# Kernel optimization log

Measured on AMD Instinct MI355X. Metric: run time of the kernel, lower is better.

Reference implementation:

```python
import jax, jax.numpy as jnp
import numpy as np

N_NODES = 50000
N_EDGES = 800000
D = 128
N_GRAPHS = 64
N_CLASSES = 10


def setup_inputs() -> dict:
    key = jax.random.key(0)
    ks = jax.random.split(key, 10)
    x = jax.random.normal(ks[0], (N_NODES, D), dtype=jnp.float32)
    edge_index = jax.random.randint(ks[1], (2, N_EDGES), 0, N_NODES, dtype=jnp.int64)
    batch = jnp.sort(jax.random.randint(ks[2], (N_NODES,), 0, N_GRAPHS, dtype=jnp.int64))
    s = 1.0 / np.sqrt(D)
    W1a = jax.random.uniform(ks[3], (D, D), jnp.float32, -s, s)
    W1b = jax.random.uniform(ks[4], (D, D), jnp.float32, -s, s)
    W2a = jax.random.uniform(ks[5], (D, D), jnp.float32, -s, s)
    W2b = jax.random.uniform(ks[6], (D, D), jnp.float32, -s, s)
    Wfc = jax.random.uniform(ks[7], (D, N_CLASSES), jnp.float32, -s, s)
    return {
        "x": x, "edge_index": edge_index, "batch": batch,
        "W1a": W1a, "b1a": jnp.zeros((D,), jnp.float32),
        "W1b": W1b, "b1b": jnp.zeros((D,), jnp.float32),
        "W2a": W2a, "b2a": jnp.zeros((D,), jnp.float32),
        "W2b": W2b, "b2b": jnp.zeros((D,), jnp.float32),
        "Wfc": Wfc, "bfc": jnp.zeros((N_CLASSES,), jnp.float32),
    }


def _gin_conv(x, src, dst, Wa, ba, Wb, bb):
    # sum aggregation of neighbor messages x[src] into dst (eps = 0)
    agg = jax.ops.segment_sum(x[src], dst, num_segments=N_NODES)
    h = x + agg  # (1 + eps) * x + sum_{j->i} x_j
    h = jax.nn.relu(h @ Wa + ba)
    h = jax.nn.relu(h @ Wb + bb)
    return h


def reference(x, edge_index, batch, W1a, b1a, W1b, b1b, W2a, b2a, W2b, b2b, Wfc, bfc):
    src, dst = edge_index[0], edge_index[1]
    h = _gin_conv(x, src, dst, W1a, b1a, W1b, b1b)
    h = _gin_conv(h, src, dst, W2a, b2a, W2b, b2b)
    # global mean pool over graphs
    sums = jax.ops.segment_sum(h, batch, num_segments=N_GRAPHS)
    counts = jax.ops.segment_sum(jnp.ones((h.shape[0], 1), h.dtype), batch, num_segments=N_GRAPHS)
    pooled = sums / jnp.maximum(counts, 1.0)
    logits = pooled @ Wfc + bfc
    return jax.nn.sigmoid(logits)
```

## Files before the change

### kernel.cpp

```cpp
#include <hip/hip_runtime.h>

#define NN 50000
#define NE 800000
#define DF 128
#define NG 64
#define NC 10
#define NBK 98
#define PART_CHUNK 4096
#define PART_GRID 196
#define ACAP 12288
#define FINE_CAP 12288
#define RT 136

typedef short bf16x8 __attribute__((ext_vector_type(8)));
typedef float f32x4  __attribute__((ext_vector_type(4)));

__device__ __forceinline__ void atomAddF(float* p, float v) {
  __hip_atomic_fetch_add(p, v, __ATOMIC_RELAXED, __HIP_MEMORY_SCOPE_AGENT);
}
__device__ __forceinline__ float b2f(unsigned short u) {
  union { unsigned int i; float f; } v; v.i = (unsigned int)u << 16; return v.f;
}
__device__ __forceinline__ unsigned int f2b(float f) {
  unsigned int i = __float_as_uint(f);
  return (i + 0x7fffu + ((i >> 16) & 1u)) >> 16;
}

__global__ __launch_bounds__(256) void k_cast(const float* __restrict__ x,
                                              unsigned short* __restrict__ xb)
{
  const int i = blockIdx.x * 256 + threadIdx.x;
  if (i * 4 >= NN * DF) return;
  const float4 v = reinterpret_cast<const float4*>(x)[i];
  uint2 o;
  o.x = f2b(v.x) | (f2b(v.y) << 16);
  o.y = f2b(v.z) | (f2b(v.w) << 16);
  reinterpret_cast<uint2*>(xb)[i] = o;
}

__global__ __launch_bounds__(256) void k_prepw(const float* __restrict__ W0,
                                               const float* __restrict__ W1,
                                               const float* __restrict__ W2,
                                               const float* __restrict__ W3,
                                               unsigned short* __restrict__ Wt)
{
  const int o = blockIdx.x * 256 + threadIdx.x;
  if (o >= 4 * 2048) return;
  const int mat = o >> 11;
  const float* W = (mat == 0) ? W0 : (mat == 1) ? W1 : (mat == 2) ? W2 : W3;
  const int rem = o & 2047;
  const int n  = rem >> 4;
  const int k0 = (rem & 15) * 8;
  unsigned int u[8];
#pragma unroll
  for (int j = 0; j < 8; ++j) u[j] = f2b(W[(size_t)(k0 + j) * DF + n]);
  uint4 p;
  p.x = u[0] | (u[1] << 16);
  p.y = u[2] | (u[3] << 16);
  p.z = u[4] | (u[5] << 16);
  p.w = u[6] | (u[7] << 16);
  *reinterpret_cast<uint4*>(Wt + (size_t)mat * DF * DF + (size_t)n * DF + k0) = p;
}

__global__ __launch_bounds__(256) void k_part(const int* __restrict__ src,
                                              const int* __restrict__ dst,
                                              int* __restrict__ cnt_b,
                                              unsigned int* __restrict__ arena)
{
  __shared__ unsigned int stage[PART_CHUNK];
  __shared__ int lhist[128], lcnt[128], lcur[128], gbase[128];
  const int tid = threadIdx.x;
  const int e0  = blockIdx.x * PART_CHUNK;
  const int nE  = min(PART_CHUNK, NE - e0);

  for (int i = tid; i < 128; i += 256) lhist[i] = 0;
  __syncthreads();

  unsigned int pk[16];
  int bk[16];
#pragma unroll
  for (int i = 0; i < 16; ++i) {
    const int e = e0 + i * 256 + tid;
    if (e < NE) {
      const int d = dst[e];
      const int s = src[e];
      const int b = d >> 9;
      bk[i] = b;
      pk[i] = ((unsigned int)b << 25) | ((unsigned int)(d & 511) << 16) | (unsigned int)s;
      atomicAdd(&lhist[b], 1);
    } else {
      bk[i] = -1;
    }
  }
  __syncthreads();
  for (int i = tid; i < 128; i += 256) lcnt[i] = lhist[i];
  __syncthreads();
  for (int off = 1; off < 128; off <<= 1) {
    int v = 0;
    if (tid < 128 && tid >= off) v = lhist[tid - off];
    __syncthreads();
    if (tid < 128) lhist[tid] += v;
    __syncthreads();
  }
  if (tid < 128) lcur[tid] = lhist[tid] - lcnt[tid];
  __syncthreads();
#pragma unroll
  for (int i = 0; i < 16; ++i) {
    if (bk[i] >= 0) {
      const int pos = atomicAdd(&lcur[bk[i]], 1);
      stage[pos] = pk[i];
    }
  }
  __syncthreads();
  if (tid < NBK) {
    const int c = lcnt[tid];
    if (c > 0) gbase[tid] = atomicAdd(&cnt_b[tid], c);
  }
  __syncthreads();
  for (int idx = tid; idx < nE; idx += 256) {
    const unsigned int p = stage[idx];
    const int b = (int)(p >> 25);
    const int loff = lhist[b] - lcnt[b];
    arena[(size_t)b * ACAP + gbase[b] + (idx - loff)] = p;
  }
}

__global__ __launch_bounds__(128) void k_bscan(const int* __restrict__ cnt_b,
                                               int* __restrict__ base_b,
                                               int* __restrict__ rs)
{
  __shared__ int sm[128];
  const int t = threadIdx.x;
  const int v = (t < NBK) ? cnt_b[t] : 0;
  sm[t] = v;
  __syncthreads();
  for (int off = 1; off < 128; off <<= 1) {
    int u = (t >= off) ? sm[t - off] : 0;
    __syncthreads();
    sm[t] += u;
    __syncthreads();
  }
  base_b[t] = sm[t] - v;
  if (t == NBK - 1) rs[NN] = sm[t];
}

__global__ __launch_bounds__(256) void k_fine(const unsigned int* __restrict__ arena,
                                              const int* __restrict__ cnt_b,
                                              const int* __restrict__ base_b,
                                              int* __restrict__ rs,
                                              int* __restrict__ es)
{
  __shared__ int hist[512], offs[512], pairs[256];
  __shared__ unsigned short les[FINE_CAP];
  const int tid   = threadIdx.x;
  const int b     = blockIdx.x;
  const int cnt   = cnt_b[b];
  const int wbase = base_b[b];
  const int nbase = b << 9;
  const int nwin  = min(512, NN - nbase);
  const unsigned int* ap = arena + (size_t)b * ACAP;

  for (int i = tid; i < 512; i += 256) hist[i] = 0;
  __syncthreads();
  for (int idx = tid; idx < cnt; idx += 256)
    atomicAdd(&hist[(ap[idx] >> 16) & 511], 1);
  __syncthreads();
  const int s0 = hist[2 * tid];
  const int s1 = hist[2 * tid + 1];
  pairs[tid] = s0 + s1;
  __syncthreads();
  for (int off = 1; off < 256; off <<= 1) {
    int u = (tid >= off) ? pairs[tid - off] : 0;
    __syncthreads();
    pairs[tid] += u;
    __syncthreads();
  }
  const int ep = pairs[tid] - s0 - s1;
  offs[2 * tid]     = ep;
  offs[2 * tid + 1] = ep + s0;
  __syncthreads();
  for (int i = tid; i < nwin; i += 256) rs[nbase + i] = wbase + offs[i];
  __syncthreads();
  if (cnt <= FINE_CAP) {
    for (int idx = tid; idx < cnt; idx += 256) {
      const unsigned int p = ap[idx];
      const int pos = atomicAdd(&offs[(p >> 16) & 511], 1);
      les[pos] = (unsigned short)(p & 0xffffu);
    }
    __syncthreads();
    for (int i = tid; i < cnt; i += 256) es[wbase + i] = (int)les[i];
  } else {
    for (int idx = tid; idx < cnt; idx += 256) {
      const unsigned int p = ap[idx];
      const int pos = atomicAdd(&offs[(p >> 16) & 511], 1);
      es[wbase + pos] = (int)(p & 0xffffu);
    }
  }
}

__global__ __launch_bounds__(256) void k_gather(const unsigned short* __restrict__ feat,
                                                unsigned short* __restrict__ outp,
                                                const int* __restrict__ rs,
                                                const int* __restrict__ es)
{
  const int wid  = (blockIdx.x * 256 + threadIdx.x) >> 6;
  const int lane = threadIdx.x & 63;
  if (wid >= NN) return;
  const int beg = rs[wid];
  const int end = rs[wid + 1];
  const int off = lane * 2;

  const unsigned int self = *reinterpret_cast<const unsigned int*>(feat + (size_t)wid * DF + off);
  float ax = b2f(self & 0xffff), ay = b2f(self >> 16);
  int j = beg;
  while (j < end && (j & 3)) {
    const unsigned int u = *reinterpret_cast<const unsigned int*>(feat + (size_t)es[j] * DF + off);
    ax += b2f(u & 0xffff);
    ay += b2f(u >> 16);
    ++j;
  }
  for (; j + 3 < end; j += 4) {
    const int4 e4 = *reinterpret_cast<const int4*>(es + j);
    const unsigned int u0 = *reinterpret_cast<const unsigned int*>(feat + (size_t)e4.x * DF + off);
    const unsigned int u1 = *reinterpret_cast<const unsigned int*>(feat + (size_t)e4.y * DF + off);
    const unsigned int u2 = *reinterpret_cast<const unsigned int*>(feat + (size_t)e4.z * DF + off);
    const unsigned int u3 = *reinterpret_cast<const unsigned int*>(feat + (size_t)e4.w * DF + off);
    ax += b2f(u0 & 0xffff) + b2f(u1 & 0xffff) + b2f(u2 & 0xffff) + b2f(u3 & 0xffff);
    ay += b2f(u0 >> 16)    + b2f(u1 >> 16)    + b2f(u2 >> 16)    + b2f(u3 >> 16);
  }
  for (; j < end; ++j) {
    const unsigned int u = *reinterpret_cast<const unsigned int*>(feat + (size_t)es[j] * DF + off);
    ax += b2f(u & 0xffff);
    ay += b2f(u >> 16);
  }
  const unsigned int o = f2b(ax) | (f2b(ay) << 16);
  *reinterpret_cast<unsigned int*>(outp + (size_t)wid * DF + off) = o;
}

__global__ __launch_bounds__(256) void k_gemm2(const unsigned short* __restrict__ Ab,
                                               const unsigned short* __restrict__ Wta,
                                               const float* __restrict__ ba,
                                               const unsigned short* __restrict__ Wtb,
                                               const float* __restrict__ bb,
                                               unsigned short* __restrict__ outb, int M)
{
  __shared__ unsigned short WbL[128 * 128];
  __shared__ unsigned short hL[4][16 * RT];
  const int tid  = threadIdx.x;
  const int lane = tid & 63;
  const int w    = tid >> 6;
  const int col  = lane & 15;
  const int kq   = lane >> 4;

  for (int i = tid; i < 2048; i += 256) {
    const int n = i >> 4, kb = i & 15;
    const int kbp = (kb + n) & 15;
    *reinterpret_cast<uint4*>(&WbL[n * 128 + kbp * 8]) =
        *reinterpret_cast<const uint4*>(&Wtb[(size_t)n * 128 + kb * 8]);
  }

  bf16x8 wfa[8][4];
#pragma unroll
  for (int nf = 0; nf < 8; ++nf)
#pragma unroll
    for (int s = 0; s < 4; ++s)
      wfa[nf][s] = *reinterpret_cast<const bf16x8*>(
          Wta + (size_t)(nf * 16 + col) * DF + s * 32 + kq * 8);

  __syncthreads();

  unsigned short* hw = &hL[w][0];
  const int rbase = blockIdx.x * 256;

  int m = rbase + w * 16 + col;
  int mld = (m < M) ? m : (M - 1);
  bf16x8 bc[4];
#pragma unroll
  for (int s = 0; s < 4; ++s)
    bc[s] = *reinterpret_cast<const bf16x8*>(Ab + (size_t)mld * DF + s * 32 + kq * 8);

#pragma unroll
  for (int t = 0; t < 4; ++t) {
    bf16x8 bn[4];
    if (t < 3) {
      const int m2 = rbase + (t + 1) * 64 + w * 16 + col;
      const int mld2 = (m2 < M) ? m2 : (M - 1);
#pragma unroll
      for (int s = 0; s < 4; ++s)
        bn[s] = *reinterpret_cast<const bf16x8*>(Ab + (size_t)mld2 * DF + s * 32 + kq * 8);
    }
    f32x4 acc[8];
#pragma unroll
    for (int nf = 0; nf < 8; ++nf) acc[nf] = (f32x4){0.f, 0.f, 0.f, 0.f};
#pragma unroll
    for (int s = 0; s < 4; ++s)
#pragma unroll
      for (int nf = 0; nf < 8; ++nf)
        acc[nf] = __builtin_amdgcn_mfma_f32_16x16x32_bf16(wfa[nf][s], bc[s], acc[nf], 0, 0, 0);
#pragma unroll
    for (int nf = 0; nf < 8; ++nf) {
      const float4 bv = *reinterpret_cast<const float4*>(ba + nf * 16 + kq * 4);
      uint2 pk;
      pk.x = f2b(fmaxf(acc[nf][0] + bv.x, 0.f)) | (f2b(fmaxf(acc[nf][1] + bv.y, 0.f)) << 16);
      pk.y = f2b(fmaxf(acc[nf][2] + bv.z, 0.f)) | (f2b(fmaxf(acc[nf][3] + bv.w, 0.f)) << 16);
      *reinterpret_cast<uint2*>(&hw[col * RT + nf * 16 + kq * 4]) = pk;
    }
    asm volatile("s_waitcnt lgkmcnt(0)" ::: "memory");
    __builtin_amdgcn_sched_barrier(0);
    f32x4 acc2[8];
#pragma unroll
    for (int nf = 0; nf < 8; ++nf) acc2[nf] = (f32x4){0.f, 0.f, 0.f, 0.f};
#pragma unroll
    for (int s = 0; s < 4; ++s) {
      const bf16x8 hb = *reinterpret_cast<const bf16x8*>(&hw[col * RT + s * 32 + kq * 8]);
#pragma unroll
      for (int nf = 0; nf < 8; ++nf) {
        const int kbp = (s * 4 + kq + col) & 15;
        const bf16x8 wb = *reinterpret_cast<const bf16x8*>(&WbL[(nf * 16 + col) * 128 + kbp * 8]);
        acc2[nf] = __builtin_amdgcn_mfma_f32_16x16x32_bf16(wb, hb, acc2[nf], 0, 0, 0);
      }
    }
    if (m < M) {
#pragma unroll
      for (int nf = 0; nf < 8; ++nf) {
        const float4 bv = *reinterpret_cast<const float4*>(bb + nf * 16 + kq * 4);
        ushort4 p;
        p.x = (unsigned short)f2b(fmaxf(acc2[nf][0] + bv.x, 0.f));
        p.y = (unsigned short)f2b(fmaxf(acc2[nf][1] + bv.y, 0.f));
        p.z = (unsigned short)f2b(fmaxf(acc2[nf][2] + bv.z, 0.f));
        p.w = (unsigned short)f2b(fmaxf(acc2[nf][3] + bv.w, 0.f));
        *reinterpret_cast<ushort4*>(outb + (size_t)m * DF + nf * 16 + kq * 4) = p;
      }
    }
#pragma unroll
    for (int s = 0; s < 4; ++s) bc[s] = bn[s];
    m = rbase + (t + 1) * 64 + w * 16 + col;
    mld = (m < M) ? m : (M - 1);
  }
}

__global__ __launch_bounds__(256) void k_pool(const unsigned short* __restrict__ h,
                                              const int* __restrict__ batch,
                                              float* __restrict__ sums,
                                              int* __restrict__ cnts)
{
  const int wv   = (blockIdx.x * 256 + threadIdx.x) >> 6;
  const int lane = threadIdx.x & 63;
  const int n0 = wv * 32;
  if (n0 >= NN) return;
  const int n1 = min(n0 + 32, NN);
  const int off = lane * 2;

  const int gfirst = batch[n0];
  const int glast  = batch[n1 - 1];
  float ax = 0.f, ay = 0.f;

  if (gfirst == glast) {
#pragma unroll 4
    for (int i = n0; i < n1; ++i) {
      const unsigned int u = *reinterpret_cast<const unsigned int*>(h + (size_t)i * DF + off);
      ax += b2f(u & 0xffff);
      ay += b2f(u >> 16);
    }
    atomAddF(&sums[gfirst * DF + off],     ax);
    atomAddF(&sums[gfirst * DF + off + 1], ay);
    if (lane == 0) atomicAdd(&cnts[gfirst], n1 - n0);
  } else {
    int g = gfirst, cnt = 0;
    for (int i = n0; i < n1; ++i) {
      const int gi = batch[i];
      if (gi != g) {
        atomAddF(&sums[g * DF + off],     ax);
        atomAddF(&sums[g * DF + off + 1], ay);
        if (lane == 0) atomicAdd(&cnts[g], cnt);
        ax = 0.f; ay = 0.f; cnt = 0; g = gi;
      }
      const unsigned int u = *reinterpret_cast<const unsigned int*>(h + (size_t)i * DF + off);
      ax += b2f(u & 0xffff);
      ay += b2f(u >> 16);
      ++cnt;
    }
    atomAddF(&sums[g * DF + off],     ax);
    atomAddF(&sums[g * DF + off + 1], ay);
    if (lane == 0) atomicAdd(&cnts[g], cnt);
  }
}

__global__ __launch_bounds__(256) void k_head(const float* __restrict__ sums,
                                              const int* __restrict__ cnts,
                                              const float* __restrict__ Wfc,
                                              const float* __restrict__ bfc,
                                              float* __restrict__ out)
{
  for (int o = threadIdx.x; o < NG * NC; o += 256) {
    const int g = o / NC, c = o % NC;
    const float inv = 1.f / fmaxf((float)cnts[g], 1.f);
    float z = bfc[c];
    for (int k = 0; k < DF; ++k)
      z = fmaf(sums[g * DF + k] * inv, Wfc[k * NC + c], z);
    out[o] = 1.f / (1.f + expf(-z));
  }
}

extern "C" void kernel_launch(void* const* d_in, const int* in_sizes, int n_in,
                              void* d_out, int out_size, void* d_ws, size_t ws_size,
                              hipStream_t stream)
{
  const float* x   = (const float*)d_in[0];
  const int*   ei  = (const int*)d_in[1];
  const int* batch = (const int*)d_in[2];
  const float* W1a = (const float*)d_in[3];
  const float* b1a = (const float*)d_in[4];
  const float* W1b = (const float*)d_in[5];
  const float* b1b = (const float*)d_in[6];
  const float* W2a = (const float*)d_in[7];
  const float* b2a = (const float*)d_in[8];
  const float* W2b = (const float*)d_in[9];
  const float* b2b = (const float*)d_in[10];
  const float* Wfc = (const float*)d_in[11];
  const float* bfc = (const float*)d_in[12];
  float* out = (float*)d_out;

  const int* src = ei;
  const int* dst = ei + NE;

  unsigned short* xb = (unsigned short*)d_ws;
  unsigned short* A  = xb + (size_t)NN * DF;
  unsigned short* H  = A + (size_t)NN * DF;
  unsigned short* Wt = H + (size_t)NN * DF;
  float* sums  = (float*)(Wt + (size_t)4 * DF * DF);
  int*   cnts  = (int*)(sums + NG * DF);
  int*   cnt_b = cnts + 64;
  int*   base_b= cnt_b + 128;
  int*   rs    = base_b + 128;
  int*   es    = rs + (NN + 4);
  unsigned int* arena = (unsigned int*)(es + NE);

  unsigned short* Wt1a = Wt;
  unsigned short* Wt1b = Wt + DF * DF;
  unsigned short* Wt2a = Wt + 2 * DF * DF;
  unsigned short* Wt2b = Wt + 3 * DF * DF;

  const int gemm_grid   = (NN + 255) / 256;
  const int gather_grid = (NN * 64 + 255) / 256;
  const int pool_grid   = ((NN + 31) / 32 + 3) / 4;

  k_cast<<<(NN * DF / 4 + 255) / 256, 256, 0, stream>>>(x, xb);
  k_prepw<<<32, 256, 0, stream>>>(W1a, W1b, W2a, W2b, Wt);
  hipMemsetAsync(sums, 0, (size_t)(NG * DF + 64 + 128) * sizeof(float), stream);
  k_part<<<PART_GRID, 256, 0, stream>>>(src, dst, cnt_b, arena);
  k_bscan<<<1, 128, 0, stream>>>(cnt_b, base_b, rs);
  k_fine<<<NBK, 256, 0, stream>>>(arena, cnt_b, base_b, rs, es);

  k_gather<<<gather_grid, 256, 0, stream>>>(xb, A, rs, es);
  k_gemm2<<<gemm_grid, 256, 0, stream>>>(A, Wt1a, b1a, Wt1b, b1b, A, NN);

  k_gather<<<gather_grid, 256, 0, stream>>>(A, H, rs, es);
  k_gemm2<<<gemm_grid, 256, 0, stream>>>(H, Wt2a, b2a, Wt2b, b2b, H, NN);

  k_pool<<<pool_grid, 256, 0, stream>>>(H, batch, sums, cnts);
  k_head<<<1, 256, 0, stream>>>(sums, cnts, Wfc, bfc, out);
}
```

Baseline: 203.5 us.

## Sort CSR edges by source within each node and store indices as ushort

```diff
diff --git a/kernel.cpp b/kernel.cpp
--- a/kernel.cpp
+++ b/kernel.cpp
@@ -148,10 +148,11 @@
                                               const int* __restrict__ cnt_b,
                                               const int* __restrict__ base_b,
                                               int* __restrict__ rs,
-                                              int* __restrict__ es)
-{
-  __shared__ int hist[512], offs[512], pairs[256];
+                                              unsigned short* __restrict__ es)
+{
   __shared__ unsigned short les[FINE_CAP];
+  __shared__ int bins[4096];
+  __shared__ int partials[256];
   const int tid   = threadIdx.x;
   const int b     = blockIdx.x;
   const int cnt   = cnt_b[b];
@@ -160,40 +161,51 @@
   const int nwin  = min(512, NN - nbase);
   const unsigned int* ap = arena + (size_t)b * ACAP;
 
-  for (int i = tid; i < 512; i += 256) hist[i] = 0;
-  __syncthreads();
-  for (int idx = tid; idx < cnt; idx += 256)
-    atomicAdd(&hist[(ap[idx] >> 16) & 511], 1);
-  __syncthreads();
-  const int s0 = hist[2 * tid];
-  const int s1 = hist[2 * tid + 1];
-  pairs[tid] = s0 + s1;
+  for (int i = tid; i < 4096; i += 256) bins[i] = 0;
+  __syncthreads();
+  for (int idx = tid; idx < cnt; idx += 256) {
+    const unsigned int p = ap[idx];
+    const int key = (int)(((p >> 16) & 511) << 3) | (int)((p & 0xffffu) >> 13);
+    atomicAdd(&bins[key], 1);
+  }
+  __syncthreads();
+  const int b16 = tid * 16;
+  int sum = 0;
+#pragma unroll
+  for (int k = 0; k < 16; ++k) sum += bins[b16 + k];
+  partials[tid] = sum;
   __syncthreads();
   for (int off = 1; off < 256; off <<= 1) {
-    int u = (tid >= off) ? pairs[tid - off] : 0;
-    __syncthreads();
-    pairs[tid] += u;
-    __syncthreads();
-  }
-  const int ep = pairs[tid] - s0 - s1;
-  offs[2 * tid]     = ep;
-  offs[2 * tid + 1] = ep + s0;
-  __syncthreads();
-  for (int i = tid; i < nwin; i += 256) rs[nbase + i] = wbase + offs[i];
+    int u = (tid >= off) ? partials[tid - off] : 0;
+    __syncthreads();
+    partials[tid] += u;
+    __syncthreads();
+  }
+  int run = partials[tid] - sum;
+#pragma unroll
+  for (int k = 0; k < 16; ++k) {
+    const int v = bins[b16 + k];
+    bins[b16 + k] = run;
+    run += v;
+  }
+  __syncthreads();
+  for (int i = tid; i < nwin; i += 256) rs[nbase + i] = wbase + bins[i << 3];
   __syncthreads();
   if (cnt <= FINE_CAP) {
     for (int idx = tid; idx < cnt; idx += 256) {
       const unsigned int p = ap[idx];
-      const int pos = atomicAdd(&offs[(p >> 16) & 511], 1);
+      const int key = (int)(((p >> 16) & 511) << 3) | (int)((p & 0xffffu) >> 13);
+      const int pos = atomicAdd(&bins[key], 1);
       les[pos] = (unsigned short)(p & 0xffffu);
     }
     __syncthreads();
-    for (int i = tid; i < cnt; i += 256) es[wbase + i] = (int)les[i];
+    for (int i = tid; i < cnt; i += 256) es[wbase + i] = les[i];
   } else {
     for (int idx = tid; idx < cnt; idx += 256) {
       const unsigned int p = ap[idx];
-      const int pos = atomicAdd(&offs[(p >> 16) & 511], 1);
-      es[wbase + pos] = (int)(p & 0xffffu);
+      const int key = (int)(((p >> 16) & 511) << 3) | (int)((p & 0xffffu) >> 13);
+      const int pos = atomicAdd(&bins[key], 1);
+      es[wbase + pos] = (unsigned short)(p & 0xffffu);
     }
   }
 }
@@ -201,7 +213,7 @@
 __global__ __launch_bounds__(256) void k_gather(const unsigned short* __restrict__ feat,
                                                 unsigned short* __restrict__ outp,
                                                 const int* __restrict__ rs,
-                                                const int* __restrict__ es)
+                                                const unsigned short* __restrict__ es)
 {
   const int wid  = (blockIdx.x * 256 + threadIdx.x) >> 6;
   const int lane = threadIdx.x & 63;
@@ -214,22 +226,26 @@
   float ax = b2f(self & 0xffff), ay = b2f(self >> 16);
   int j = beg;
   while (j < end && (j & 3)) {
-    const unsigned int u = *reinterpret_cast<const unsigned int*>(feat + (size_t)es[j] * DF + off);
+    const int s = es[j];
+    const unsigned int u = *reinterpret_cast<const unsigned int*>(feat + (size_t)s * DF + off);
     ax += b2f(u & 0xffff);
     ay += b2f(u >> 16);
     ++j;
   }
   for (; j + 3 < end; j += 4) {
-    const int4 e4 = *reinterpret_cast<const int4*>(es + j);
-    const unsigned int u0 = *reinterpret_cast<const unsigned int*>(feat + (size_t)e4.x * DF + off);
-    const unsigned int u1 = *reinterpret_cast<const unsigned int*>(feat + (size_t)e4.y * DF + off);
-    const unsigned int u2 = *reinterpret_cast<const unsigned int*>(feat + (size_t)e4.z * DF + off);
-    const unsigned int u3 = *reinterpret_cast<const unsigned int*>(feat + (size_t)e4.w * DF + off);
+    const uint2 e4 = *reinterpret_cast<const uint2*>(es + j);
+    const int s0 = (int)(e4.x & 0xffffu), s1 = (int)(e4.x >> 16);
+    const int s2 = (int)(e4.y & 0xffffu), s3 = (int)(e4.y >> 16);
+    const unsigned int u0 = *reinterpret_cast<const unsigned int*>(feat + (size_t)s0 * DF + off);
+    const unsigned int u1 = *reinterpret_cast<const unsigned int*>(feat + (size_t)s1 * DF + off);
+    const unsigned int u2 = *reinterpret_cast<const unsigned int*>(feat + (size_t)s2 * DF + off);
+    const unsigned int u3 = *reinterpret_cast<const unsigned int*>(feat + (size_t)s3 * DF + off);
     ax += b2f(u0 & 0xffff) + b2f(u1 & 0xffff) + b2f(u2 & 0xffff) + b2f(u3 & 0xffff);
     ay += b2f(u0 >> 16)    + b2f(u1 >> 16)    + b2f(u2 >> 16)    + b2f(u3 >> 16);
   }
   for (; j < end; ++j) {
-    const unsigned int u = *reinterpret_cast<const unsigned int*>(feat + (size_t)es[j] * DF + off);
+    const int s = es[j];
+    const unsigned int u = *reinterpret_cast<const unsigned int*>(feat + (size_t)s * DF + off);
     ax += b2f(u & 0xffff);
     ay += b2f(u >> 16);
   }
@@ -433,7 +449,7 @@
   int*   cnt_b = cnts + 64;
   int*   base_b= cnt_b + 128;
   int*   rs    = base_b + 128;
-  int*   es    = rs + (NN + 4);
+  unsigned short* es = (unsigned short*)(rs + (NN + 4));
   unsigned int* arena = (unsigned int*)(es + NE);
 
   unsigned short* Wt1a = Wt;
```

New measurement: 205.0 us. Within noise of the previous version (+0.7%).
